# Optimization experiments

Measured on AMD Instinct MI355X. Metric: run time of the kernel, lower is better.

Reference implementation:

```python
import jax, jax.numpy as jnp
import numpy as np

E = 8      # num_experts
D = 1024   # input_size
H = 1024   # hidden_size
K = 2      # top_k
B = 2
S = 1024


def setup_inputs() -> dict:
    key = jax.random.key(0)
    ks = jax.random.split(key, 5)
    x = jax.random.normal(ks[0], (B, S, D), dtype=jnp.float32)
    p = jax.random.uniform(ks[1], (B * S, K), dtype=jnp.float32)
    expert_p = p / p.sum(axis=-1, keepdims=True)            # normalized top-k gates
    expert_idxs = jax.random.randint(ks[2], (B * S, K), 0, E)
    W1 = jax.random.normal(ks[3], (E, D, 2 * H), dtype=jnp.float32) * (D ** -0.5)
    W2 = jax.random.normal(ks[4], (E, H, D), dtype=jnp.float32) * (H ** -0.5)
    return {"x": x, "expert_p": expert_p, "expert_idxs": expert_idxs, "W1": W1, "W2": W2}


def reference(x, expert_p, expert_idxs, W1, W2):
    x_shape = x.shape
    xf = x.reshape(-1, x_shape[-1])                 # [N, D]
    n_tok = xf.shape[0]
    k = expert_idxs.shape[-1]
    x_pair = jnp.repeat(xf, k, axis=0)              # [N*K, D] token replicated per expert slot
    idx = expert_idxs.reshape(-1)                   # [N*K]
    p = expert_p.reshape(-1)                        # [N*K]
    y_pair = jnp.zeros((n_tok * k, x_shape[-1]), dtype=x.dtype)
    # loop over fixed small expert count; masked dense GEMM per expert
    for e in range(W1.shape[0]):
        m = (idx == e).astype(x.dtype)[:, None]     # [N*K, 1]
        hg = (x_pair * m) @ W1[e]                   # [N*K, 2H]
        h, g = jnp.split(hg, 2, axis=-1)            # chunk(2): (h, gates)
        a = jax.nn.silu(g) * h                      # SiLU-gated GLU
        y_pair = y_pair + (a @ W2[e]) * m           # [N*K, D]
    # combine: weight each pair by its gate prob and sum over top_k slots
    y = (y_pair * p[:, None]).reshape(n_tok, k, -1).sum(axis=1)
    return y.reshape(x_shape)
```

## Files before the change

### kernel.cpp

```cpp
#include <hip/hip_runtime.h>


typedef __bf16 bf16x8 __attribute__((ext_vector_type(8)));
typedef __bf16 bf16x4 __attribute__((ext_vector_type(4)));
typedef float  f32x4  __attribute__((ext_vector_type(4)));

#define NPAIR 4096
#define NTOK  2048
#define DDIM  1024
#define HDIM  1024
#define NEXP  8

#define ORDER_I   64
#define XB_OFF    (24576)
#define W1T_OFF   (XB_OFF + 4194304)
#define W2T_OFF   (W1T_OFF + 33554432)
#define ACT_OFF   (W2T_OFF + 16777216)

#define GLOAD_LDS16(g, l) \
    __builtin_amdgcn_global_load_lds( \
        (const __attribute__((address_space(1))) void*)(g), \
        (__attribute__((address_space(3))) void*)(l), 16, 0, 0)

__device__ __forceinline__ void tcvt64(const float* __restrict__ s,
                                       __bf16* __restrict__ d,
                                       int R, int C, int k0, int c0,
                                       float (*tt)[65], int tid) {
#pragma unroll
    for (int p = 0; p < 4; p++) {
        int kr = p * 16 + (tid >> 4);
        int nc = (tid & 15) * 4;
        *(float4*)&tt[kr][nc] = *(const float4*)(s + (size_t)(k0 + kr) * C + c0 + nc);
    }
    __syncthreads();
#pragma unroll
    for (int p = 0; p < 2; p++) {
        int cid = p * 256 + tid;
        int n = cid >> 3, kc = cid & 7;
        bf16x8 o;
#pragma unroll
        for (int j = 0; j < 8; j++) o[j] = (__bf16)tt[kc * 8 + j][n];
        *(bf16x8*)(d + (size_t)(c0 + n) * R + k0 + kc * 8) = o;
    }
}

__global__ __launch_bounds__(256) void prep_kernel(const float* __restrict__ x,
                                                   const float* __restrict__ W1,
                                                   const int* __restrict__ idx,
                                                   int* __restrict__ wsi,
                                                   __bf16* __restrict__ xb,
                                                   __bf16* __restrict__ w1t) {
    __shared__ float tt[64][65];
    __shared__ int cnt[NEXP];
    __shared__ int sbase, scur;
    const int b = blockIdx.x;
    const int tid = threadIdx.x;
    if (b < 4096) {
        int e = b >> 9, t2 = b & 511;
        int k0 = (t2 & 15) * 64, c0 = (t2 >> 4) * 64;
        tcvt64(W1 + (size_t)e * DDIM * 2 * HDIM, w1t + (size_t)e * 2 * HDIM * DDIM,
               DDIM, 2 * HDIM, k0, c0, tt, tid);
    } else if (b < 6144) {
        int i = (b - 4096) * 1024 + tid * 4;
        float4 v = *(const float4*)(x + i);
        bf16x4 o;
        o[0] = (__bf16)v.x; o[1] = (__bf16)v.y; o[2] = (__bf16)v.z; o[3] = (__bf16)v.w;
        *(bf16x4*)(xb + i) = o;
    } else {
        const int e = b - 6144;
        if (tid < NEXP) cnt[tid] = 0;
        if (tid == 0) scur = 0;
        __syncthreads();
        for (int i = tid; i < NPAIR; i += 256) atomicAdd(&cnt[idx[i] & 7], 1);
        __syncthreads();
        if (tid == 0) {
            int off = 0;
            for (int e2 = 0; e2 < NEXP; e2++) {
                if (e2 == e) { wsi[e] = cnt[e]; wsi[8 + e] = off; sbase = off; }
                off += (cnt[e2] + 127) & ~127;
            }
        }
        __syncthreads();
        for (int i = tid; i < NPAIR; i += 256) {
            if ((idx[i] & 7) == e) {
                int s = atomicAdd(&scur, 1);
                wsi[ORDER_I + sbase + s] = i;
            }
        }
    }
}

__global__ __launch_bounds__(256) void gemm1_kernel(const __bf16* __restrict__ xb,
                                                    const __bf16* __restrict__ w1t,
                                                    const int* __restrict__ wsi,
                                                    __bf16* __restrict__ act,
                                                    const float* __restrict__ W2,
                                                    __bf16* __restrict__ w2t,
                                                    float* __restrict__ out) {
    __shared__ __align__(16) char smem[49152];
    const int tid = threadIdx.x;
    const int z = blockIdx.z;

    if (z >= 8) {
        int aux = (z - 8) * 1024 + blockIdx.y * 16 + blockIdx.x;
        if (aux < 2048) {
            int e = aux >> 8, t2 = aux & 255;
            int k0 = (t2 & 15) * 64, c0 = (t2 >> 4) * 64;
            tcvt64(W2 + (size_t)e * HDIM * DDIM, w2t + (size_t)e * DDIM * HDIM,
                   HDIM, DDIM, k0, c0, (float (*)[65])smem, tid);
        } else if (aux < 2560) {
            int zb = aux - 2048;
            float4 z4 = {0.f, 0.f, 0.f, 0.f};
            int b4 = zb * 4096;
#pragma unroll
            for (int j = 0; j < 4; j++)
                *(float4*)(out + b4 + j * 1024 + tid * 4) = z4;
        }
        return;
    }

    const int e = z;
    const int cnt = wsi[e];
    const int m0 = blockIdx.y * 64;
    if (m0 >= cnt) return;
    const int base = wsi[8 + e];
    const int n0 = blockIdx.x * 64;
    const int* order = wsi + ORDER_I;
    const __bf16* w1e = w1t + (size_t)e * 2048 * 1024;

    const int lane = tid & 63, w = tid >> 6;
    const int lm = lane & 15, q = lane >> 4;
    const int wm = w & 1, wn = w >> 1;
    const int x7 = lm & 7;
    const int sw0 = (q ^ x7) * 16;
    const int sw1 = ((4 + q) ^ x7) * 16;

    const __bf16* ga[2];
    const __bf16* gb[4];
#pragma unroll
    for (int j = 0; j < 2; j++) {
        int c = j * 256 + tid;
        int r = c >> 3;
        int ks = ((c & 7) ^ (r & 7)) * 8;
        int m = m0 + r; if (m >= cnt) m = cnt - 1;
        int tok = order[base + m] >> 1;
        ga[j] = xb + (size_t)tok * DDIM + ks;
    }
#pragma unroll
    for (int j = 0; j < 4; j++) {
        int c = j * 256 + tid;
        int r = c >> 3;
        int ks = ((c & 7) ^ (r & 7)) * 8;
        int half = r >> 6, rr = r & 63;
        int rb = (rr < 32) ? (n0 + half * 32 + rr)
                           : (HDIM + n0 + half * 32 + (rr - 32));
        gb[j] = w1e + (size_t)rb * DDIM + ks;
    }

    f32x4 acc[2][4];
#pragma unroll
    for (int mt = 0; mt < 2; mt++)
#pragma unroll
        for (int nt = 0; nt < 4; nt++) acc[mt][nt] = (f32x4){0.f, 0.f, 0.f, 0.f};

#pragma unroll
    for (int j = 0; j < 2; j++) {
        GLOAD_LDS16(ga[j], smem + (j * 256 + tid) * 16);
        ga[j] += 64;
    }
#pragma unroll
    for (int j = 0; j < 4; j++) {
        GLOAD_LDS16(gb[j], smem + 8192 + (j * 256 + tid) * 16);
        gb[j] += 64;
    }

    for (int t = 0; t < 16; ++t) {
        char* cbase = smem + (t & 1) * 24576;
        if (t < 15) {
            char* nbase = smem + ((t + 1) & 1) * 24576;
#pragma unroll
            for (int j = 0; j < 2; j++) {
                GLOAD_LDS16(ga[j], nbase + (j * 256 + tid) * 16);
                ga[j] += 64;
            }
#pragma unroll
            for (int j = 0; j < 4; j++) {
                GLOAD_LDS16(gb[j], nbase + 8192 + (j * 256 + tid) * 16);
                gb[j] += 64;
            }
            asm volatile("s_waitcnt vmcnt(6)" ::: "memory");
        } else {
            asm volatile("s_waitcnt vmcnt(0)" ::: "memory");
        }
        __builtin_amdgcn_s_barrier();
        __builtin_amdgcn_sched_barrier(0);
        __bf16 (*As)[64] = (__bf16 (*)[64])cbase;
        __bf16 (*Bs)[64] = (__bf16 (*)[64])(cbase + 8192);
#pragma unroll
        for (int kh = 0; kh < 2; kh++) {
            const int sw = kh ? sw1 : sw0;
            bf16x8 af[2];
#pragma unroll
            for (int mt = 0; mt < 2; mt++)
                af[mt] = *(const bf16x8*)((const char*)&As[wm * 32 + mt * 16 + lm][0] + sw);
            __builtin_amdgcn_s_setprio(1);
#pragma unroll
            for (int nt = 0; nt < 4; nt++) {
                bf16x8 bfr = *(const bf16x8*)((const char*)&Bs[wn * 64 + nt * 16 + lm][0] + sw);
#pragma unroll
                for (int mt = 0; mt < 2; mt++)
                    acc[mt][nt] = __builtin_amdgcn_mfma_f32_16x16x32_bf16(af[mt], bfr, acc[mt][nt], 0, 0, 0);
            }
            __builtin_amdgcn_s_setprio(0);
        }
        __builtin_amdgcn_sched_barrier(0);
        __builtin_amdgcn_s_barrier();
    }

#pragma unroll
    for (int mt = 0; mt < 2; mt++) {
        int mbase = m0 + wm * 32 + mt * 16 + q * 4;
#pragma unroll
        for (int ntp = 0; ntp < 2; ntp++) {
            int col = n0 + wn * 32 + ntp * 16 + lm;
#pragma unroll
            for (int r = 0; r < 4; r++) {
                int m = mbase + r;
                if (m < cnt) {
                    float h = acc[mt][ntp][r];
                    float g = acc[mt][ntp + 2][r];
                    float a = h * (g / (1.f + __expf(-g)));
                    act[(size_t)(base + m) * HDIM + col] = (__bf16)a;
                }
            }
        }
    }
}

__global__ __launch_bounds__(256) void gemm2_kernel(const __bf16* __restrict__ act,
                                                    const __bf16* __restrict__ w2t,
                                                    const int* __restrict__ wsi,
                                                    const float* __restrict__ p,
                                                    float* __restrict__ out) {
    const int e = blockIdx.z;
    const int cnt = wsi[e];
    const int m0 = blockIdx.y * 64;
    if (m0 >= cnt) return;
    const int base = wsi[8 + e];
    const int n0 = blockIdx.x * 64;
    const int* order = wsi + ORDER_I;
    const __bf16* w2e = w2t + (size_t)e * 1024 * 1024;

    __shared__ __align__(16) char smem[32768];

    const int tid = threadIdx.x;
    const int lane = tid & 63, w = tid >> 6;
    const int lm = lane & 15, q = lane >> 4;
    const int wm = w & 1, wn = w >> 1;
    const int x7 = lm & 7;
    const int sw0 = (q ^ x7) * 16;
    const int sw1 = ((4 + q) ^ x7) * 16;

    const __bf16* ga[2];
    const __bf16* gb[2];
#pragma unroll
    for (int j = 0; j < 2; j++) {
        int c = j * 256 + tid;
        int r = c >> 3;
        int ks = ((c & 7) ^ (r & 7)) * 8;
        ga[j] = act + (size_t)(base + m0 + r) * HDIM + ks;
        gb[j] = w2e + (size_t)(n0 + r) * HDIM + ks;
    }

    f32x4 acc[2][2];
#pragma unroll
    for (int mt = 0; mt < 2; mt++)
#pragma unroll
        for (int nt = 0; nt < 2; nt++) acc[mt][nt] = (f32x4){0.f, 0.f, 0.f, 0.f};

#pragma unroll
    for (int j = 0; j < 2; j++) {
        GLOAD_LDS16(ga[j], smem + (j * 256 + tid) * 16);
        GLOAD_LDS16(gb[j], smem + 8192 + (j * 256 + tid) * 16);
        ga[j] += 64; gb[j] += 64;
    }

    for (int t = 0; t < 16; ++t) {
        char* cbase = smem + (t & 1) * 16384;
        if (t < 15) {
            char* nbase = smem + ((t + 1) & 1) * 16384;
#pragma unroll
            for (int j = 0; j < 2; j++) {
                GLOAD_LDS16(ga[j], nbase + (j * 256 + tid) * 16);
                GLOAD_LDS16(gb[j], nbase + 8192 + (j * 256 + tid) * 16);
                ga[j] += 64; gb[j] += 64;
            }
            asm volatile("s_waitcnt vmcnt(4)" ::: "memory");
        } else {
            asm volatile("s_waitcnt vmcnt(0)" ::: "memory");
        }
        __builtin_amdgcn_s_barrier();
        __builtin_amdgcn_sched_barrier(0);
        __bf16 (*As)[64] = (__bf16 (*)[64])cbase;
        __bf16 (*Bs)[64] = (__bf16 (*)[64])(cbase + 8192);
#pragma unroll
        for (int kh = 0; kh < 2; kh++) {
            const int sw = kh ? sw1 : sw0;
            bf16x8 af[2];
#pragma unroll
            for (int mt = 0; mt < 2; mt++)
                af[mt] = *(const bf16x8*)((const char*)&As[wm * 32 + mt * 16 + lm][0] + sw);
            __builtin_amdgcn_s_setprio(1);
#pragma unroll
            for (int nt = 0; nt < 2; nt++) {
                bf16x8 bfr = *(const bf16x8*)((const char*)&Bs[wn * 32 + nt * 16 + lm][0] + sw);
#pragma unroll
                for (int mt = 0; mt < 2; mt++)
                    acc[mt][nt] = __builtin_amdgcn_mfma_f32_16x16x32_bf16(af[mt], bfr, acc[mt][nt], 0, 0, 0);
            }
            __builtin_amdgcn_s_setprio(0);
        }
        __builtin_amdgcn_sched_barrier(0);
        __builtin_amdgcn_s_barrier();
    }

    int pi[2][4];
    float pw[2][4];
#pragma unroll
    for (int mt = 0; mt < 2; mt++)
#pragma unroll
        for (int r = 0; r < 4; r++) {
            int gm = m0 + wm * 32 + mt * 16 + q * 4 + r;
            if (gm < cnt) {
                int pr = order[base + gm];
                pi[mt][r] = pr;
                pw[mt][r] = p[pr];
            } else pi[mt][r] = -1;
        }
#pragma unroll
    for (int mt = 0; mt < 2; mt++)
#pragma unroll
        for (int nt = 0; nt < 2; nt++) {
            int col = n0 + wn * 32 + nt * 16 + lm;
#pragma unroll
            for (int r = 0; r < 4; r++) {
                if (pi[mt][r] >= 0) {
                    int tok = pi[mt][r] >> 1;
                    atomicAdd(out + (size_t)tok * DDIM + col, pw[mt][r] * acc[mt][nt][r]);
                }
            }
        }
}

extern "C" void kernel_launch(void* const* d_in, const int* in_sizes, int n_in,
                              void* d_out, int out_size, void* d_ws, size_t ws_size,
                              hipStream_t stream) {
    (void)in_sizes; (void)n_in; (void)out_size; (void)ws_size;
    const float* x   = (const float*)d_in[0];
    const float* p   = (const float*)d_in[1];
    const int* eidx  = (const int*)d_in[2];
    const float* W1  = (const float*)d_in[3];
    const float* W2  = (const float*)d_in[4];
    float* out = (float*)d_out;

    char* ws = (char*)d_ws;
    int* wsi     = (int*)ws;
    __bf16* xb   = (__bf16*)(ws + XB_OFF);
    __bf16* w1t  = (__bf16*)(ws + W1T_OFF);
    __bf16* w2t  = (__bf16*)(ws + W2T_OFF);
    __bf16* act  = (__bf16*)(ws + ACT_OFF);

    prep_kernel<<<6152, 256, 0, stream>>>(x, W1, eidx, wsi, xb, w1t);
    gemm1_kernel<<<dim3(16, 64, 11), 256, 0, stream>>>(xb, w1t, wsi, act, W2, w2t, out);
    gemm2_kernel<<<dim3(16, 64, NEXP), 256, 0, stream>>>(act, w2t, wsi, p, out);
}
```

Measured before the change: 200.5 us.

## Rewrite weight transpose-convert with LDS async loads, bigger tiles, triple-buffer gemm2

The fp32-to-bf16 transpose of W1 and W2 now loads 64x128 tiles straight into LDS with global_load_lds and converts them through register vectors, halving the number of transpose blocks. The x conversion now uses wider 8-element chunks per thread. Zeroing the output moves from gemm1's auxiliary z-slices into prep_kernel, so gemm1 needs only one extra z-slice. gemm2 switches from double to triple buffering of LDS with deeper prefetch, which raises LDS use to 48KB and may reduce occupancy.

After: 205.5 us. +2.5%, slower.

```diff
diff --git a/kernel.cpp b/kernel.cpp
--- a/kernel.cpp
+++ b/kernel.cpp
@@ -22,25 +22,28 @@
         (const __attribute__((address_space(1))) void*)(g), \
         (__attribute__((address_space(3))) void*)(l), 16, 0, 0)
 
-__device__ __forceinline__ void tcvt64(const float* __restrict__ s,
-                                       __bf16* __restrict__ d,
-                                       int R, int C, int k0, int c0,
-                                       float (*tt)[65], int tid) {
-#pragma unroll
-    for (int p = 0; p < 4; p++) {
-        int kr = p * 16 + (tid >> 4);
-        int nc = (tid & 15) * 4;
-        *(float4*)&tt[kr][nc] = *(const float4*)(s + (size_t)(k0 + kr) * C + c0 + nc);
+__device__ __forceinline__ void tcvt2(const float* __restrict__ s,
+                                      __bf16* __restrict__ d,
+                                      int R, int C, int k0, int c0,
+                                      float* tt, int tid) {
+#pragma unroll
+    for (int j = 0; j < 8; j++) {
+        int c = j * 256 + tid;
+        int row = c >> 5, col = (c & 31) * 4;
+        GLOAD_LDS16(s + (size_t)(k0 + row) * C + c0 + col, (char*)tt + c * 16);
     }
     __syncthreads();
-#pragma unroll
-    for (int p = 0; p < 2; p++) {
-        int cid = p * 256 + tid;
-        int n = cid >> 3, kc = cid & 7;
+    const int a = tid >> 5, b = tid & 31;
+    f32x4 v[8];
+#pragma unroll
+    for (int jj = 0; jj < 8; jj++)
+        v[jj] = *(const f32x4*)(tt + (8 * a + jj) * 128 + 4 * b);
+#pragma unroll
+    for (int ii = 0; ii < 4; ii++) {
         bf16x8 o;
 #pragma unroll
-        for (int j = 0; j < 8; j++) o[j] = (__bf16)tt[kc * 8 + j][n];
-        *(bf16x8*)(d + (size_t)(c0 + n) * R + k0 + kc * 8) = o;
+        for (int jj = 0; jj < 8; jj++) o[jj] = (__bf16)v[jj][ii];
+        *(bf16x8*)(d + (size_t)(c0 + 4 * b + ii) * R + k0 + 8 * a) = o;
     }
 }
 
@@ -49,25 +52,39 @@
                                                    const int* __restrict__ idx,
                                                    int* __restrict__ wsi,
                                                    __bf16* __restrict__ xb,
-                                                   __bf16* __restrict__ w1t) {
-    __shared__ float tt[64][65];
+                                                   __bf16* __restrict__ w1t,
+                                                   float* __restrict__ out) {
+    __shared__ __align__(16) float tt[64 * 128];
     __shared__ int cnt[NEXP];
     __shared__ int sbase, scur;
     const int b = blockIdx.x;
     const int tid = threadIdx.x;
-    if (b < 4096) {
-        int e = b >> 9, t2 = b & 511;
-        int k0 = (t2 & 15) * 64, c0 = (t2 >> 4) * 64;
-        tcvt64(W1 + (size_t)e * DDIM * 2 * HDIM, w1t + (size_t)e * 2 * HDIM * DDIM,
-               DDIM, 2 * HDIM, k0, c0, tt, tid);
-    } else if (b < 6144) {
-        int i = (b - 4096) * 1024 + tid * 4;
-        float4 v = *(const float4*)(x + i);
-        bf16x4 o;
-        o[0] = (__bf16)v.x; o[1] = (__bf16)v.y; o[2] = (__bf16)v.z; o[3] = (__bf16)v.w;
-        *(bf16x4*)(xb + i) = o;
+    if (b < 2048) {
+        int e = b >> 8, t2 = b & 255;
+        int k0 = (t2 & 15) * 64, c0 = (t2 >> 4) * 128;
+        tcvt2(W1 + (size_t)e * DDIM * 2 * HDIM, w1t + (size_t)e * 2 * HDIM * DDIM,
+              DDIM, 2 * HDIM, k0, c0, tt, tid);
+    } else if (b < 2304) {
+        size_t base = (size_t)(b - 2048) * 8192 + tid * 8;
+#pragma unroll
+        for (int j = 0; j < 4; j++) {
+            const float* sp = x + base + j * 2048;
+            f32x4 v0 = *(const f32x4*)sp;
+            f32x4 v1 = *(const f32x4*)(sp + 4);
+            bf16x8 o;
+            o[0] = (__bf16)v0[0]; o[1] = (__bf16)v0[1]; o[2] = (__bf16)v0[2]; o[3] = (__bf16)v0[3];
+            o[4] = (__bf16)v1[0]; o[5] = (__bf16)v1[1]; o[6] = (__bf16)v1[2]; o[7] = (__bf16)v1[3];
+            *(bf16x8*)(xb + base + j * 2048) = o;
+        }
+    } else if (b < 2816) {
+        int zb = b - 2304;
+        float4 z4 = {0.f, 0.f, 0.f, 0.f};
+        int b4 = zb * 4096;
+#pragma unroll
+        for (int j = 0; j < 4; j++)
+            *(float4*)(out + b4 + j * 1024 + tid * 4) = z4;
     } else {
-        const int e = b - 6144;
+        const int e = b - 2816;
         if (tid < NEXP) cnt[tid] = 0;
         if (tid == 0) scur = 0;
         __syncthreads();
@@ -95,27 +112,17 @@
                                                     const int* __restrict__ wsi,
                                                     __bf16* __restrict__ act,
                                                     const float* __restrict__ W2,
-                                                    __bf16* __restrict__ w2t,
-                                                    float* __restrict__ out) {
+                                                    __bf16* __restrict__ w2t) {
     __shared__ __align__(16) char smem[49152];
     const int tid = threadIdx.x;
     const int z = blockIdx.z;
 
     if (z >= 8) {
-        int aux = (z - 8) * 1024 + blockIdx.y * 16 + blockIdx.x;
-        if (aux < 2048) {
-            int e = aux >> 8, t2 = aux & 255;
-            int k0 = (t2 & 15) * 64, c0 = (t2 >> 4) * 64;
-            tcvt64(W2 + (size_t)e * HDIM * DDIM, w2t + (size_t)e * DDIM * HDIM,
-                   HDIM, DDIM, k0, c0, (float (*)[65])smem, tid);
-        } else if (aux < 2560) {
-            int zb = aux - 2048;
-            float4 z4 = {0.f, 0.f, 0.f, 0.f};
-            int b4 = zb * 4096;
-#pragma unroll
-            for (int j = 0; j < 4; j++)
-                *(float4*)(out + b4 + j * 1024 + tid * 4) = z4;
-        }
+        int aux = blockIdx.y * 16 + blockIdx.x;
+        int e = aux >> 7, t2 = aux & 127;
+        int k0 = (t2 & 15) * 64, c0 = (t2 >> 4) * 128;
+        tcvt2(W2 + (size_t)e * HDIM * DDIM, w2t + (size_t)e * DDIM * HDIM,
+              HDIM, DDIM, k0, c0, (float*)smem, tid);
         return;
     }
 
@@ -251,7 +258,7 @@
     const int* order = wsi + ORDER_I;
     const __bf16* w2e = w2t + (size_t)e * 1024 * 1024;
 
-    __shared__ __align__(16) char smem[32768];
+    __shared__ __align__(16) char smem[49152];
 
     const int tid = threadIdx.x;
     const int lane = tid & 63, w = tid >> 6;
@@ -279,22 +286,28 @@
         for (int nt = 0; nt < 2; nt++) acc[mt][nt] = (f32x4){0.f, 0.f, 0.f, 0.f};
 
 #pragma unroll
-    for (int j = 0; j < 2; j++) {
-        GLOAD_LDS16(ga[j], smem + (j * 256 + tid) * 16);
-        GLOAD_LDS16(gb[j], smem + 8192 + (j * 256 + tid) * 16);
-        ga[j] += 64; gb[j] += 64;
+    for (int t = 0; t < 2; ++t) {
+        char* nb = smem + t * 16384;
+#pragma unroll
+        for (int j = 0; j < 2; j++) {
+            GLOAD_LDS16(ga[j], nb + (j * 256 + tid) * 16);
+            GLOAD_LDS16(gb[j], nb + 8192 + (j * 256 + tid) * 16);
+            ga[j] += 64; gb[j] += 64;
+        }
     }
 
     for (int t = 0; t < 16; ++t) {
-        char* cbase = smem + (t & 1) * 16384;
-        if (t < 15) {
-            char* nbase = smem + ((t + 1) & 1) * 16384;
+        char* cbase = smem + (t % 3) * 16384;
+        if (t < 14) {
+            char* nbase = smem + ((t + 2) % 3) * 16384;
 #pragma unroll
             for (int j = 0; j < 2; j++) {
                 GLOAD_LDS16(ga[j], nbase + (j * 256 + tid) * 16);
                 GLOAD_LDS16(gb[j], nbase + 8192 + (j * 256 + tid) * 16);
                 ga[j] += 64; gb[j] += 64;
             }
+            asm volatile("s_waitcnt vmcnt(8)" ::: "memory");
+        } else if (t == 14) {
             asm volatile("s_waitcnt vmcnt(4)" ::: "memory");
         } else {
             asm volatile("s_waitcnt vmcnt(0)" ::: "memory");
@@ -370,7 +383,7 @@
     __bf16* w2t  = (__bf16*)(ws + W2T_OFF);
     __bf16* act  = (__bf16*)(ws + ACT_OFF);
 
-    prep_kernel<<<6152, 256, 0, stream>>>(x, W1, eidx, wsi, xb, w1t);
-    gemm1_kernel<<<dim3(16, 64, 11), 256, 0, stream>>>(xb, w1t, wsi, act, W2, w2t, out);
+    prep_kernel<<<2824, 256, 0, stream>>>(x, W1, eidx, wsi, xb, w1t, out);
+    gemm1_kernel<<<dim3(16, 64, 9), 256, 0, stream>>>(xb, w1t, wsi, act, W2, w2t);
     gemm2_kernel<<<dim3(16, 64, NEXP), 256, 0, stream>>>(act, w2t, wsi, p, out);
 }
```
